# Kernel optimization log

Measured on AMD Instinct MI355X. Metric: run time of the kernel, lower is better.

Reference implementation:

```python
import jax, jax.numpy as jnp
import numpy as np

N_NODES = 100000
N_EDGES = 1600000
HIDDEN = 128
DENSE = 64
N_GRAPHS = 512


def setup_inputs() -> dict:
    key = jax.random.key(0)
    ks = jax.random.split(key, 12)
    x = jax.random.normal(ks[0], (N_NODES, 3), dtype=jnp.float32)
    edge_index = jax.random.randint(ks[1], (2, N_EDGES), 0, N_NODES, dtype=jnp.int64)
    batch = jnp.sort(jax.random.randint(ks[2], (N_NODES,), 0, N_GRAPHS, dtype=jnp.int64))
    def lin(k, fan_in, fan_out):
        s = 1.0 / np.sqrt(fan_in)
        kw, kb = jax.random.split(k)
        W = jax.random.uniform(kw, (fan_in, fan_out), jnp.float32, -s, s)
        b = jax.random.uniform(kb, (fan_out,), jnp.float32, -s, s)
        return W, b
    W0, b0 = lin(ks[3], 3, HIDDEN)
    W1, b1 = lin(ks[4], HIDDEN, HIDDEN)
    W2, b2 = lin(ks[5], HIDDEN, HIDDEN)
    Wf1, bf1 = lin(ks[6], HIDDEN, DENSE)
    Wf2, bf2 = lin(ks[7], DENSE, 1)
    return {"x": x, "edge_index": edge_index, "batch": batch,
            "W0": W0, "b0": b0, "W1": W1, "b1": b1, "W2": W2, "b2": b2,
            "Wf1": Wf1, "bf1": bf1, "Wf2": Wf2, "bf2": bf2}


def reference(x, edge_index, batch, W0, b0, W1, b1, W2, b2, Wf1, bf1, Wf2, bf2):
    N = x.shape[0]
    loop = jnp.arange(N, dtype=edge_index.dtype)
    src = jnp.concatenate([edge_index[0], loop])  # [E+N] with self-loops
    dst = jnp.concatenate([edge_index[1], loop])
    deg = jax.ops.segment_sum(jnp.ones_like(dst, dtype=x.dtype), dst, num_segments=N)
    dis = jax.lax.rsqrt(jnp.maximum(deg, 1.0))  # D^{-1/2}; self-loops => deg >= 1
    norm = dis[src] * dis[dst]  # [E+N]

    def gcn_conv(h, W, b):
        h = h @ W  # transform first (PyG GCNConv)
        msg = h[src] * norm[:, None]  # gather + edge-wise scale
        return jax.ops.segment_sum(msg, dst, num_segments=N) + b  # scatter-add

    h = jax.nn.relu(gcn_conv(x, W0, b0))
    h = jax.nn.relu(gcn_conv(h, W1, b1))
    h = jax.nn.relu(gcn_conv(h, W2, b2))

    # global mean pool over graphs
    counts = jax.ops.segment_sum(jnp.ones((N,), h.dtype), batch, num_segments=N_GRAPHS)
    pooled = jax.ops.segment_sum(h, batch, num_segments=N_GRAPHS)
    pooled = pooled / jnp.maximum(counts, 1.0)[:, None]  # [G, HIDDEN]

    out = jax.nn.relu(pooled @ Wf1 + bf1)
    return out @ Wf2 + bf2  # [G, 1]
```

## Files before the change

### kernel.cpp

```cpp
#include <hip/hip_runtime.h>

#define HID 128
#define ELLW 64

#define NBINS 400
#define BINCAP 38
#define CHUNK_I4 1024
#define BKCAP 5120
#define OVF_CAP 16384

typedef _Float16 half8 __attribute__((ext_vector_type(8)));
typedef float f32x4 __attribute__((ext_vector_type(4)));
struct alignas(8) H4v { _Float16 x, y, z, w; };


__global__ void k_zero_ints(int* p, int n) {
  int i = blockIdx.x * blockDim.x + threadIdx.x;
  if (i < n) p[i] = 0;
}

__device__ __forceinline__ void bin_one(int s, int d, int* lcnt, unsigned* bins,
                                        int* ovfn, int2* ovf) {
  int b = d >> 8;
  int p = atomicAdd(&lcnt[b], 1);
  if (p < BINCAP) bins[b * BINCAP + p] = ((unsigned)s << 8) | (unsigned)(d & 255);
  else { int q = atomicAdd(ovfn, 1); if (q < OVF_CAP) ovf[q] = make_int2(s, d); }
}

__global__ __launch_bounds__(256) void k_binA(
    const int4* __restrict__ src4, const int4* __restrict__ dst4, int E4,
    int* bkcnt, unsigned* __restrict__ bk, int* ovfn, int2* __restrict__ ovf) {
  __shared__ unsigned bins[NBINS * BINCAP];
  __shared__ int lcnt[NBINS];
  __shared__ int gbase[NBINS];
  int t = threadIdx.x;
  for (int b = t; b < NBINS; b += 256) lcnt[b] = 0;
  __syncthreads();

  int i0 = blockIdx.x * CHUNK_I4;
  int i1 = min(i0 + CHUNK_I4, E4);
  for (int i = i0 + t; i < i1; i += 256) {
    int4 d = dst4[i];
    int4 s = src4[i];
    bin_one(s.x, d.x, lcnt, bins, ovfn, ovf);
    bin_one(s.y, d.y, lcnt, bins, ovfn, ovf);
    bin_one(s.z, d.z, lcnt, bins, ovfn, ovf);
    bin_one(s.w, d.w, lcnt, bins, ovfn, ovf);
  }
  __syncthreads();

  for (int b = t; b < NBINS; b += 256) gbase[b] = atomicAdd(&bkcnt[b], min(lcnt[b], BINCAP));
  __syncthreads();

  int wid = t >> 6, lane = t & 63;
  for (int b = wid; b < NBINS; b += 4) {
    int c = min(lcnt[b], BINCAP);
    if (lane < c) {
      int off = gbase[b] + lane;
      unsigned r = bins[b * BINCAP + lane];
      if (off < BKCAP) bk[(size_t)b * BKCAP + off] = r;
      else {
        int q = atomicAdd(ovfn, 1);
        if (q < OVF_CAP) ovf[q] = make_int2((int)(r >> 8), b * 256 + (int)(r & 255));
      }
    }
  }
}

__global__ void k_tail_ovf(const int* __restrict__ src, const int* __restrict__ dst,
                           int e0, int E, int* ovfn, int2* __restrict__ ovf) {
  int e = e0 + threadIdx.x;
  if (e < E) {
    int q = atomicAdd(ovfn, 1);
    if (q < OVF_CAP) ovf[q] = make_int2(src[e], dst[e]);
  }
}


__global__ __launch_bounds__(256) void k_ell_build2(
    const unsigned* __restrict__ bk, const int* __restrict__ bkcnt,
    int* __restrict__ ell, int* __restrict__ cnt, int N) {
  int b = blockIdx.x;
  int t = threadIdx.x;
  __shared__ int lcnt[256];
  lcnt[t] = 0;
  __syncthreads();
  int n = bkcnt[b]; if (n > BKCAP) n = BKCAP;
  const unsigned* my = bk + (size_t)b * BKCAP;
  for (int k = t; k < n; k += 256) {
    unsigned r = my[k];
    int d0 = (int)(r & 255);
    int s = (int)(r >> 8);
    int p = atomicAdd(&lcnt[d0], 1);
    if (p < ELLW) ell[(size_t)(b * 256 + d0) * ELLW + p] = s;
  }
  __syncthreads();
  int node = b * 256 + t;
  if (node < N) cnt[node] = lcnt[t];
}

__global__ void k_ovf_build(const int2* __restrict__ ovf, const int* __restrict__ ovfn,
                            int* cnt, int* ell) {
  int n = *ovfn; if (n > OVF_CAP) n = OVF_CAP;
  for (int k = threadIdx.x; k < n; k += blockDim.x) {
    int2 e = ovf[k];
    int p = atomicAdd(&cnt[e.y], 1);
    if (p < ELLW) ell[(size_t)e.y * ELLW + p] = e.x;
  }
}

__global__ void k_fill_ell1(const int* __restrict__ src, const int* __restrict__ dst,
                            int* cnt, int* ell, int E) {
  int e = blockIdx.x * blockDim.x + threadIdx.x;
  if (e < E) {
    int d = dst[e];
    int p = atomicAdd(&cnt[d], 1);
    if (p < ELLW) ell[(size_t)d * ELLW + p] = src[e];
  }
}


__global__ void k_dis_prepx(const int* __restrict__ cnt, const float* __restrict__ x,
                            float* __restrict__ dis, float4* __restrict__ x4, int N) {
  int i = blockIdx.x * blockDim.x + threadIdx.x;
  if (i >= N) return;
  float s = rsqrtf((float)(cnt[i] + 1));
  dis[i] = s;
  x4[i] = make_float4(s * x[i * 3 + 0], s * x[i * 3 + 1], s * x[i * 3 + 2], 0.f);
}


__global__ void k_agg3(const float4* __restrict__ x4, const int* __restrict__ ell,
                       const int* __restrict__ cnt, const float* __restrict__ dis,
                       float4* __restrict__ z4, int N) {
  int i = blockIdx.x * blockDim.x + threadIdx.x;
  if (i >= N) return;
  float4 a = x4[i];
  int c = cnt[i]; if (c > ELLW) c = ELLW;
  const int* row = &ell[(size_t)i * ELLW];
  int k = 0;
  for (; k + 4 <= c; k += 4) {
    int4 s4 = *(const int4*)(row + k);
    float4 v0 = x4[s4.x], v1 = x4[s4.y], v2 = x4[s4.z], v3 = x4[s4.w];
    a.x += (v0.x + v1.x) + (v2.x + v3.x);
    a.y += (v0.y + v1.y) + (v2.y + v3.y);
    a.z += (v0.z + v1.z) + (v2.z + v3.z);
  }
  for (; k < c; ++k) {
    float4 v = x4[row[k]];
    a.x += v.x; a.y += v.y; a.z += v.z;
  }
  float s = dis[i];
  z4[i] = make_float4(s * a.x, s * a.y, s * a.z, 0.f);
}


__global__ void k_prep_w16x2(const float* __restrict__ W1, const float* __restrict__ W2,
                             _Float16* __restrict__ Wt1, _Float16* __restrict__ Wt2) {
  int idx = blockIdx.x * blockDim.x + threadIdx.x;
  if (idx >= 2 * HID * HID) return;
  int which = idx >> 14;
  int r = idx & (HID * HID - 1);
  int k = r >> 7, n = r & 127;
  const float* W = which ? W2 : W1;
  _Float16* Wt = which ? Wt2 : Wt1;
  Wt[n * HID + k] = (_Float16)W[r];
}


__global__ __launch_bounds__(256) void k_l01(
    const float4* __restrict__ z4, const float* __restrict__ W0,
    const float* __restrict__ b0, const _Float16* __restrict__ wt1,
    const float* __restrict__ dis, _Float16* __restrict__ G, int N) {
  __shared__ _Float16 hs[64][136];
  int t = threadIdx.x;
  int base = blockIdx.x * 64;

  {
    int r = t >> 2;
    int c0 = (t & 3) * 32;
    int row = base + r;
    float4 z = make_float4(0.f, 0.f, 0.f, 0.f);
    if (row < N) z = z4[row];
#pragma unroll
    for (int c = 0; c < 32; c += 4) {
      int cc = c0 + c;
      float4 w0 = *(const float4*)&W0[0 * HID + cc];
      float4 w1 = *(const float4*)&W0[1 * HID + cc];
      float4 w2 = *(const float4*)&W0[2 * HID + cc];
      float4 bb = *(const float4*)&b0[cc];
      H4v o;
      o.x = (_Float16)fmaxf(z.x * w0.x + z.y * w1.x + z.z * w2.x + bb.x, 0.f);
      o.y = (_Float16)fmaxf(z.x * w0.y + z.y * w1.y + z.z * w2.y + bb.y, 0.f);
      o.z = (_Float16)fmaxf(z.x * w0.z + z.y * w1.z + z.z * w2.z + bb.z, 0.f);
      o.w = (_Float16)fmaxf(z.x * w0.w + z.y * w1.w + z.z * w2.w + bb.w, 0.f);
      *(H4v*)&hs[r][cc] = o;
    }
  }
  __syncthreads();

  int w = t >> 6, lane = t & 63;
  int kg = lane >> 4, ccol = lane & 15;
  int lrow = w * 16 + ccol;

  f32x4 acc[8];
#pragma unroll
  for (int nt = 0; nt < 8; ++nt) acc[nt] = (f32x4){0.f, 0.f, 0.f, 0.f};

#pragma unroll
  for (int kt = 0; kt < 4; ++kt) {
    half8 a = *(const half8*)&hs[lrow][kg * 8 + kt * 32];
#pragma unroll
    for (int nt = 0; nt < 8; ++nt) {
      half8 b = *(const half8*)(wt1 + (size_t)(nt * 16 + ccol) * HID + kg * 8 + kt * 32);
      acc[nt] = __builtin_amdgcn_mfma_f32_16x16x32_f16(a, b, acc[nt], 0, 0, 0);
    }
  }

#pragma unroll
  for (int j = 0; j < 4; ++j) {
    int row = base + w * 16 + kg * 4 + j;
    if (row < N) {
      float s = dis[row];
#pragma unroll
      for (int nt = 0; nt < 8; ++nt) {
        G[(size_t)row * HID + nt * 16 + ccol] = (_Float16)(s * acc[nt][j]);
      }
    }
  }
}


__global__ __launch_bounds__(256) void k_g1(
    const _Float16* __restrict__ g16, const int* __restrict__ ell,
    const int* __restrict__ cnt, const float* __restrict__ dis,
    const float* __restrict__ b, _Float16* __restrict__ q1, int N) {
  int tid = blockIdx.x * blockDim.x + threadIdx.x;
  int i = tid >> 4;
  int q = tid & 15;
  if (i >= N) return;
  const _Float16* gq = g16 + q * 8;

  float acc[8];
  half8 sv = *(const half8*)(gq + (size_t)i * HID);
#pragma unroll
  for (int j = 0; j < 8; ++j) acc[j] = (float)sv[j];

  int c = cnt[i]; if (c > ELLW) c = ELLW;
  const int* row = ell + (size_t)i * ELLW;
  int k = 0;
  for (; k + 8 <= c; k += 8) {
    int4 sa = *(const int4*)(row + k);
    int4 sb = *(const int4*)(row + k + 4);
    half8 v0 = *(const half8*)(gq + (size_t)sa.x * HID);
    half8 v1 = *(const half8*)(gq + (size_t)sa.y * HID);
    half8 v2 = *(const half8*)(gq + (size_t)sa.z * HID);
    half8 v3 = *(const half8*)(gq + (size_t)sa.w * HID);
    half8 v4 = *(const half8*)(gq + (size_t)sb.x * HID);
    half8 v5 = *(const half8*)(gq + (size_t)sb.y * HID);
    half8 v6 = *(const half8*)(gq + (size_t)sb.z * HID);
    half8 v7 = *(const half8*)(gq + (size_t)sb.w * HID);
#pragma unroll
    for (int j = 0; j < 8; ++j) {
      float p01 = (float)v0[j] + (float)v1[j];
      float p23 = (float)v2[j] + (float)v3[j];
      float p45 = (float)v4[j] + (float)v5[j];
      float p67 = (float)v6[j] + (float)v7[j];
      acc[j] += (p01 + p23) + (p45 + p67);
    }
  }
  for (; k + 4 <= c; k += 4) {
    int4 s4 = *(const int4*)(row + k);
    half8 v0 = *(const half8*)(gq + (size_t)s4.x * HID);
    half8 v1 = *(const half8*)(gq + (size_t)s4.y * HID);
    half8 v2 = *(const half8*)(gq + (size_t)s4.z * HID);
    half8 v3 = *(const half8*)(gq + (size_t)s4.w * HID);
#pragma unroll
    for (int j = 0; j < 8; ++j)
      acc[j] += ((float)v0[j] + (float)v1[j]) + ((float)v2[j] + (float)v3[j]);
  }
  for (; k < c; ++k) {
    half8 v = *(const half8*)(gq + (size_t)row[k] * HID);
#pragma unroll
    for (int j = 0; j < 8; ++j) acc[j] += (float)v[j];
  }

  float sc = dis[i];
  half8 o;
#pragma unroll
  for (int j = 0; j < 8; ++j) {
    float bb = b[q * 8 + j];
    o[j] = (_Float16)(sc * fmaxf(sc * acc[j] + bb, 0.f));
  }
  *(half8*)(q1 + (size_t)i * HID + q * 8) = o;
}


__global__ __launch_bounds__(256) void k_gpool2(
    const _Float16* __restrict__ q1, const int* __restrict__ ell,
    const int* __restrict__ cnt, const float* __restrict__ dis,
    const float* __restrict__ b2, const _Float16* __restrict__ wt2,
    const int* __restrict__ batch, float* __restrict__ pool, int N) {
  __shared__ _Float16 hs[16][136];
  int t = threadIdx.x;
  int base = blockIdx.x * 16;
  int gi = t >> 4, q = t & 15;
  int i = base + gi;

  if (i < N) {
    const _Float16* gq = q1 + q * 8;
    float acc[8];
    half8 sv = *(const half8*)(gq + (size_t)i * HID);
#pragma unroll
    for (int j = 0; j < 8; ++j) acc[j] = (float)sv[j];

    int c = cnt[i]; if (c > ELLW) c = ELLW;
    const int* row = ell + (size_t)i * ELLW;
    int k = 0;
    for (; k + 8 <= c; k += 8) {
      int4 sa = *(const int4*)(row + k);
      int4 sb = *(const int4*)(row + k + 4);
      half8 v0 = *(const half8*)(gq + (size_t)sa.x * HID);
      half8 v1 = *(const half8*)(gq + (size_t)sa.y * HID);
      half8 v2 = *(const half8*)(gq + (size_t)sa.z * HID);
      half8 v3 = *(const half8*)(gq + (size_t)sa.w * HID);
      half8 v4 = *(const half8*)(gq + (size_t)sb.x * HID);
      half8 v5 = *(const half8*)(gq + (size_t)sb.y * HID);
      half8 v6 = *(const half8*)(gq + (size_t)sb.z * HID);
      half8 v7 = *(const half8*)(gq + (size_t)sb.w * HID);
#pragma unroll
      for (int j = 0; j < 8; ++j) {
        float p01 = (float)v0[j] + (float)v1[j];
        float p23 = (float)v2[j] + (float)v3[j];
        float p45 = (float)v4[j] + (float)v5[j];
        float p67 = (float)v6[j] + (float)v7[j];
        acc[j] += (p01 + p23) + (p45 + p67);
      }
    }
    for (; k + 4 <= c; k += 4) {
      int4 s4 = *(const int4*)(row + k);
      half8 v0 = *(const half8*)(gq + (size_t)s4.x * HID);
      half8 v1 = *(const half8*)(gq + (size_t)s4.y * HID);
      half8 v2 = *(const half8*)(gq + (size_t)s4.z * HID);
      half8 v3 = *(const half8*)(gq + (size_t)s4.w * HID);
#pragma unroll
      for (int j = 0; j < 8; ++j)
        acc[j] += ((float)v0[j] + (float)v1[j]) + ((float)v2[j] + (float)v3[j]);
    }
    for (; k < c; ++k) {
      half8 v = *(const half8*)(gq + (size_t)row[k] * HID);
#pragma unroll
      for (int j = 0; j < 8; ++j) acc[j] += (float)v[j];
    }

    float sc = dis[i];
    half8 o;
#pragma unroll
    for (int j = 0; j < 8; ++j) o[j] = (_Float16)(sc * acc[j]);
    *(half8*)&hs[gi][q * 8] = o;
  } else {
    half8 zo;
#pragma unroll
    for (int j = 0; j < 8; ++j) zo[j] = (_Float16)0.f;
    *(half8*)&hs[gi][q * 8] = zo;
  }
  __syncthreads();

  int w = t >> 6, lane = t & 63;
  int kg = lane >> 4, rloc = lane & 15;
  f32x4 acc2[2];
  acc2[0] = (f32x4){0.f, 0.f, 0.f, 0.f};
  acc2[1] = (f32x4){0.f, 0.f, 0.f, 0.f};

#pragma unroll
  for (int kt = 0; kt < 4; ++kt) {
    half8 a = *(const half8*)&hs[rloc][kg * 8 + kt * 32];
#pragma unroll
    for (int ntl = 0; ntl < 2; ++ntl) {
      int n = (2 * w + ntl) * 16 + rloc;
      half8 bf = *(const half8*)(wt2 + (size_t)n * HID + kg * 8 + kt * 32);
      acc2[ntl] = __builtin_amdgcn_mfma_f32_16x16x32_f16(a, bf, acc2[ntl], 0, 0, 0);
    }
  }

  float v2[2][4];
#pragma unroll
  for (int ntl = 0; ntl < 2; ++ntl) {
    int col = (2 * w + ntl) * 16 + rloc;
    float bb = b2[col];
#pragma unroll
    for (int j = 0; j < 4; ++j) v2[ntl][j] = fmaxf(acc2[ntl][j] + bb, 0.f);
  }
  int brow[4];
#pragma unroll
  for (int j = 0; j < 4; ++j) {
    int row = base + kg * 4 + j;
    brow[j] = (row < N) ? batch[row] : -1;
  }
  int g0 = batch[base];
  int lastr = base + 15; if (lastr >= N) lastr = N - 1;
  int g1 = batch[lastr];

  for (int s = g0; s <= g1; ++s) {
#pragma unroll
    for (int ntl = 0; ntl < 2; ++ntl) {
      float p = 0.f;
#pragma unroll
      for (int j = 0; j < 4; ++j) p += (brow[j] == s) ? v2[ntl][j] : 0.f;
      p += __shfl_xor(p, 16);
      p += __shfl_xor(p, 32);
      if (kg == 0 && p != 0.f) {
        atomicAdd(&pool[s * HID + (2 * w + ntl) * 16 + rloc], p);
      }
    }
  }
}


__device__ __forceinline__ int lower_bound_i(const int* __restrict__ a, int n, int v) {
  int lo = 0, hi = n;
  while (lo < hi) {
    int m = (lo + hi) >> 1;
    if (a[m] < v) lo = m + 1; else hi = m;
  }
  return lo;
}

__global__ __launch_bounds__(64) void k_mlp512(
    const float* __restrict__ pool, const int* __restrict__ batch, int N,
    const float* __restrict__ Wf1, const float* __restrict__ bf1,
    const float* __restrict__ Wf2, const float* __restrict__ bf2,
    float* __restrict__ out) {
  int g = blockIdx.x;
  int lane = threadIdx.x;
  int lo = lower_bound_i(batch, N, g);
  int hi = lower_bound_i(batch, N, g + 1);
  float inv = 1.0f / fmaxf((float)(hi - lo), 1.0f);

  __shared__ float p[128];
  p[lane] = pool[g * HID + lane] * inv;
  p[lane + 64] = pool[g * HID + 64 + lane] * inv;
  __syncthreads();

  float a = bf1[lane];
  for (int k = 0; k < 128; ++k) a += p[k] * Wf1[k * 64 + lane];
  a = fmaxf(a, 0.f);
  float prod = a * Wf2[lane];
#pragma unroll
  for (int off = 32; off; off >>= 1) prod += __shfl_down(prod, off);
  if (lane == 0) out[g] = prod + bf2[0];
}


static inline size_t align256(size_t x) { return (x + 255) & ~(size_t)255; }

extern "C" void kernel_launch(void* const* d_in, const int* in_sizes, int n_in,
                              void* d_out, int out_size, void* d_ws, size_t ws_size,
                              hipStream_t stream) {
  const float* x = (const float*)d_in[0];
  const int* ei = (const int*)d_in[1];
  const int* batch = (const int*)d_in[2];
  const float* W0 = (const float*)d_in[3];
  const float* b0 = (const float*)d_in[4];
  const float* W1 = (const float*)d_in[5];
  const float* b1 = (const float*)d_in[6];
  const float* W2 = (const float*)d_in[7];
  const float* b2 = (const float*)d_in[8];
  const float* Wf1 = (const float*)d_in[9];
  const float* bf1 = (const float*)d_in[10];
  const float* Wf2 = (const float*)d_in[11];
  const float* bf2 = (const float*)d_in[12];
  float* out = (float*)d_out;

  const int N = in_sizes[0] / 3;
  const int E = in_sizes[1] / 2;
  const int Gn = out_size;
  const int nbuk = (N + 255) >> 8;

  const int* src = ei;
  const int* dst = ei + E;

  char* ws = (char*)d_ws;
  size_t o = 0;
  int* cnt = (int*)(ws + o); o = align256(o + (size_t)N * 4);
  float* dis = (float*)(ws + o); o = align256(o + (size_t)N * 4);
  float4* x4 = (float4*)(ws + o); o = align256(o + (size_t)N * 16);
  float4* z4 = (float4*)(ws + o); o = align256(o + (size_t)N * 16);
  int* ell = (int*)(ws + o); o = align256(o + (size_t)N * ELLW * 4);
  _Float16* g16a = (_Float16*)(ws + o); o = align256(o + (size_t)N * HID * 2);
  _Float16* q1 = (_Float16*)(ws + o); o = align256(o + (size_t)N * HID * 2);
  _Float16* wt1 = (_Float16*)(ws + o); o = align256(o + (size_t)HID * HID * 2);
  _Float16* wt2 = (_Float16*)(ws + o); o = align256(o + (size_t)HID * HID * 2);
  size_t zero_base = o;
  int* bkcnt = (int*)(ws + o); o = align256(o + (size_t)(NBINS + 1) * 4);
  int* ovfn = bkcnt + NBINS;
  float* pool = (float*)(ws + o); o = align256(o + (size_t)Gn * HID * 4);
  size_t zero_bytes = o - zero_base;
  unsigned* bk = (unsigned*)(ws + o); o = align256(o + (size_t)NBINS * BKCAP * 4);
  int2* ovf = (int2*)(ws + o); o = align256(o + (size_t)OVF_CAP * 8);

  const int BS = 256;
  int gN = (N + BS - 1) / BS;
  int gN16 = (int)(((long long)N * 16 + BS - 1) / BS);
  int gW2 = (2 * HID * HID + BS - 1) / BS;
  int zn = (int)(zero_bytes / 4);

  k_zero_ints<<<(zn + BS - 1) / BS, BS, 0, stream>>>((int*)(ws + zero_base), zn);

  bool vec4ok = (E % 4 == 0) && (((uintptr_t)src & 15) == 0) && (((uintptr_t)dst & 15) == 0);
  if (nbuk <= NBINS) {
    int E4 = E / 4;
    if (E4 > 0 && vec4ok) {
      k_binA<<<(E4 + CHUNK_I4 - 1) / CHUNK_I4, 256, 0, stream>>>(
          (const int4*)src, (const int4*)dst, E4, bkcnt, bk, ovfn, ovf);
      if (E % 4) k_tail_ovf<<<1, 64, 0, stream>>>(src, dst, E4 * 4, E, ovfn, ovf);
    } else {
      k_tail_ovf<<<1, 256, 0, stream>>>(src, dst, 0, E, ovfn, ovf);
    }
    k_ell_build2<<<nbuk, 256, 0, stream>>>(bk, bkcnt, ell, cnt, N);
    k_ovf_build<<<1, 256, 0, stream>>>(ovf, ovfn, cnt, ell);
  } else {
    k_zero_ints<<<gN, BS, 0, stream>>>(cnt, N);
    k_fill_ell1<<<(E + BS - 1) / BS, BS, 0, stream>>>(src, dst, cnt, ell, E);
  }

  k_dis_prepx<<<gN, BS, 0, stream>>>(cnt, x, dis, x4, N);

  k_prep_w16x2<<<gW2, BS, 0, stream>>>(W1, W2, wt1, wt2);

  k_agg3<<<gN, BS, 0, stream>>>(x4, ell, cnt, dis, z4, N);

  k_l01<<<(N + 63) / 64, 256, 0, stream>>>(z4, W0, b0, wt1, dis, g16a, N);

  k_g1<<<gN16, BS, 0, stream>>>(g16a, ell, cnt, dis, b1, q1, N);

  k_gpool2<<<(N + 15) / 16, 256, 0, stream>>>(q1, ell, cnt, dis, b2, wt2, batch, pool, N);

  k_mlp512<<<Gn, 64, 0, stream>>>(pool, batch, N, Wf1, bf1, Wf2, bf2, out);
}
```

Measured before the change: 270.6 us.

## Fuse degree normalization into ELL build and layer-0 aggregation into k_l01

```diff
diff --git a/kernel.cpp b/kernel.cpp
--- a/kernel.cpp
+++ b/kernel.cpp
@@ -4,8 +4,8 @@
 #define ELLW 64
 
 #define NBINS 400
-#define BINCAP 38
-#define CHUNK_I4 1024
+#define BINCAP 16
+#define CHUNK_I4 512
 #define BKCAP 5120
 #define OVF_CAP 16384
 
@@ -79,7 +79,9 @@
 
 __global__ __launch_bounds__(256) void k_ell_build2(
     const unsigned* __restrict__ bk, const int* __restrict__ bkcnt,
-    int* __restrict__ ell, int* __restrict__ cnt, int N) {
+    int* __restrict__ ell, int* __restrict__ cnt,
+    const float* __restrict__ x, float* __restrict__ dis,
+    float4* __restrict__ x4, int N) {
   int b = blockIdx.x;
   int t = threadIdx.x;
   __shared__ int lcnt[256];
@@ -96,18 +98,34 @@
   }
   __syncthreads();
   int node = b * 256 + t;
-  if (node < N) cnt[node] = lcnt[t];
+  if (node < N) {
+    int c = lcnt[t];
+    cnt[node] = c;
+    float s = rsqrtf((float)(c + 1));
+    dis[node] = s;
+    x4[node] = make_float4(s * x[node * 3 + 0], s * x[node * 3 + 1],
+                           s * x[node * 3 + 2], 0.f);
+  }
 }
 
 __global__ void k_ovf_build(const int2* __restrict__ ovf, const int* __restrict__ ovfn,
-                            int* cnt, int* ell) {
+                            int* cnt, int* ell, const float* __restrict__ x,
+                            float* dis, float4* x4) {
   int n = *ovfn; if (n > OVF_CAP) n = OVF_CAP;
   for (int k = threadIdx.x; k < n; k += blockDim.x) {
     int2 e = ovf[k];
     int p = atomicAdd(&cnt[e.y], 1);
     if (p < ELLW) ell[(size_t)e.y * ELLW + p] = e.x;
   }
-}
+  __syncthreads();
+  for (int k = threadIdx.x; k < n; k += blockDim.x) {
+    int d = ovf[k].y;
+    float s = rsqrtf((float)(cnt[d] + 1));
+    dis[d] = s;
+    x4[d] = make_float4(s * x[d * 3 + 0], s * x[d * 3 + 1], s * x[d * 3 + 2], 0.f);
+  }
+}
+
 
 __global__ void k_fill_ell1(const int* __restrict__ src, const int* __restrict__ dst,
                             int* cnt, int* ell, int E) {
@@ -119,7 +137,6 @@
   }
 }
 
-
 __global__ void k_dis_prepx(const int* __restrict__ cnt, const float* __restrict__ x,
                             float* __restrict__ dis, float4* __restrict__ x4, int N) {
   int i = blockIdx.x * blockDim.x + threadIdx.x;
@@ -127,31 +144,6 @@
   float s = rsqrtf((float)(cnt[i] + 1));
   dis[i] = s;
   x4[i] = make_float4(s * x[i * 3 + 0], s * x[i * 3 + 1], s * x[i * 3 + 2], 0.f);
-}
-
-
-__global__ void k_agg3(const float4* __restrict__ x4, const int* __restrict__ ell,
-                       const int* __restrict__ cnt, const float* __restrict__ dis,
-                       float4* __restrict__ z4, int N) {
-  int i = blockIdx.x * blockDim.x + threadIdx.x;
-  if (i >= N) return;
-  float4 a = x4[i];
-  int c = cnt[i]; if (c > ELLW) c = ELLW;
-  const int* row = &ell[(size_t)i * ELLW];
-  int k = 0;
-  for (; k + 4 <= c; k += 4) {
-    int4 s4 = *(const int4*)(row + k);
-    float4 v0 = x4[s4.x], v1 = x4[s4.y], v2 = x4[s4.z], v3 = x4[s4.w];
-    a.x += (v0.x + v1.x) + (v2.x + v3.x);
-    a.y += (v0.y + v1.y) + (v2.y + v3.y);
-    a.z += (v0.z + v1.z) + (v2.z + v3.z);
-  }
-  for (; k < c; ++k) {
-    float4 v = x4[row[k]];
-    a.x += v.x; a.y += v.y; a.z += v.z;
-  }
-  float s = dis[i];
-  z4[i] = make_float4(s * a.x, s * a.y, s * a.z, 0.f);
 }
 
 
@@ -169,7 +161,8 @@
 
 
 __global__ __launch_bounds__(256) void k_l01(
-    const float4* __restrict__ z4, const float* __restrict__ W0,
+    const float4* __restrict__ x4, const int* __restrict__ ell,
+    const int* __restrict__ cnt, const float* __restrict__ W0,
     const float* __restrict__ b0, const _Float16* __restrict__ wt1,
     const float* __restrict__ dis, _Float16* __restrict__ G, int N) {
   __shared__ _Float16 hs[64][136];
@@ -177,23 +170,40 @@
   int base = blockIdx.x * 64;
 
   {
-    int r = t >> 2;
-    int c0 = (t & 3) * 32;
+    int r = t >> 2, sub = t & 3;
     int row = base + r;
-    float4 z = make_float4(0.f, 0.f, 0.f, 0.f);
-    if (row < N) z = z4[row];
-#pragma unroll
-    for (int c = 0; c < 32; c += 4) {
-      int cc = c0 + c;
+    int rc = (row < N) ? row : (N - 1);
+
+    float ax = 0.f, ay = 0.f, az = 0.f;
+    int c = cnt[rc]; if (c > ELLW) c = ELLW;
+    const int* er = ell + (size_t)rc * ELLW;
+    for (int k = sub; k < c; k += 4) {
+      float4 v = x4[er[k]];
+      ax += v.x; ay += v.y; az += v.z;
+    }
+    if (sub == 0) {
+      float4 v = x4[rc];
+      ax += v.x; ay += v.y; az += v.z;
+    }
+    ax += __shfl_xor(ax, 1); ax += __shfl_xor(ax, 2);
+    ay += __shfl_xor(ay, 1); ay += __shfl_xor(ay, 2);
+    az += __shfl_xor(az, 1); az += __shfl_xor(az, 2);
+    float s = dis[rc];
+    float zx = s * ax, zy = s * ay, zz = s * az;
+
+    int c0 = sub * 32;
+#pragma unroll
+    for (int cdx = 0; cdx < 32; cdx += 4) {
+      int cc = c0 + cdx;
       float4 w0 = *(const float4*)&W0[0 * HID + cc];
       float4 w1 = *(const float4*)&W0[1 * HID + cc];
       float4 w2 = *(const float4*)&W0[2 * HID + cc];
       float4 bb = *(const float4*)&b0[cc];
       H4v o;
-      o.x = (_Float16)fmaxf(z.x * w0.x + z.y * w1.x + z.z * w2.x + bb.x, 0.f);
-      o.y = (_Float16)fmaxf(z.x * w0.y + z.y * w1.y + z.z * w2.y + bb.y, 0.f);
-      o.z = (_Float16)fmaxf(z.x * w0.z + z.y * w1.z + z.z * w2.z + bb.z, 0.f);
-      o.w = (_Float16)fmaxf(z.x * w0.w + z.y * w1.w + z.z * w2.w + bb.w, 0.f);
+      o.x = (_Float16)fmaxf(zx * w0.x + zy * w1.x + zz * w2.x + bb.x, 0.f);
+      o.y = (_Float16)fmaxf(zx * w0.y + zy * w1.y + zz * w2.y + bb.y, 0.f);
+      o.z = (_Float16)fmaxf(zx * w0.z + zy * w1.z + zz * w2.z + bb.z, 0.f);
+      o.w = (_Float16)fmaxf(zx * w0.w + zy * w1.w + zz * w2.w + bb.w, 0.f);
       *(H4v*)&hs[r][cc] = o;
     }
   }
@@ -485,7 +495,6 @@
   int* cnt = (int*)(ws + o); o = align256(o + (size_t)N * 4);
   float* dis = (float*)(ws + o); o = align256(o + (size_t)N * 4);
   float4* x4 = (float4*)(ws + o); o = align256(o + (size_t)N * 16);
-  float4* z4 = (float4*)(ws + o); o = align256(o + (size_t)N * 16);
   int* ell = (int*)(ws + o); o = align256(o + (size_t)N * ELLW * 4);
   _Float16* g16a = (_Float16*)(ws + o); o = align256(o + (size_t)N * HID * 2);
   _Float16* q1 = (_Float16*)(ws + o); o = align256(o + (size_t)N * HID * 2);
@@ -517,20 +526,17 @@
     } else {
       k_tail_ovf<<<1, 256, 0, stream>>>(src, dst, 0, E, ovfn, ovf);
     }
-    k_ell_build2<<<nbuk, 256, 0, stream>>>(bk, bkcnt, ell, cnt, N);
-    k_ovf_build<<<1, 256, 0, stream>>>(ovf, ovfn, cnt, ell);
+    k_ell_build2<<<nbuk, 256, 0, stream>>>(bk, bkcnt, ell, cnt, x, dis, x4, N);
+    k_ovf_build<<<1, 256, 0, stream>>>(ovf, ovfn, cnt, ell, x, dis, x4);
   } else {
     k_zero_ints<<<gN, BS, 0, stream>>>(cnt, N);
     k_fill_ell1<<<(E + BS - 1) / BS, BS, 0, stream>>>(src, dst, cnt, ell, E);
-  }
-
-  k_dis_prepx<<<gN, BS, 0, stream>>>(cnt, x, dis, x4, N);
+    k_dis_prepx<<<gN, BS, 0, stream>>>(cnt, x, dis, x4, N);
+  }
 
   k_prep_w16x2<<<gW2, BS, 0, stream>>>(W1, W2, wt1, wt2);
 
-  k_agg3<<<gN, BS, 0, stream>>>(x4, ell, cnt, dis, z4, N);
-
-  k_l01<<<(N + 63) / 64, 256, 0, stream>>>(z4, W0, b0, wt1, dis, g16a, N);
+  k_l01<<<(N + 63) / 64, 256, 0, stream>>>(x4, ell, cnt, W0, b0, wt1, dis, g16a, N);
 
   k_g1<<<gN16, BS, 0, stream>>>(g16a, ell, cnt, dis, b1, q1, N);
 
```

New measurement: 273.9 us. About the same (+1.2%).
